# Kernel optimization log

Measured on AMD Instinct MI355X. Metric: run time of the kernel, lower is better.

Reference implementation:

```python
import jax, jax.numpy as jnp
import numpy as np

B, T, D = 4, 2048, 1024
H = 16
DK = D // H


def setup_inputs() -> dict:
    key = jax.random.key(0)
    k1, k2, k3, k4 = jax.random.split(key, 4)
    x = jax.random.normal(k1, (B, T, D), dtype=jnp.float32)
    prefix_lengths = jax.random.randint(k2, (B,), 0, 1024, dtype=jnp.int64)
    # torch Linear weights: [out_features, in_features], scaled like kaiming-uniform-ish
    W_qkv = jax.random.normal(k3, (3 * D, D), dtype=jnp.float32) / np.sqrt(D)
    W_o = jax.random.normal(k4, (D, D), dtype=jnp.float32) / np.sqrt(D)
    return {"x": x, "prefix_lengths": prefix_lengths, "W_qkv": W_qkv, "W_o": W_o}


def _prefix_lm_mask(seq_len, prefix_lengths):
    # True where attention is BLOCKED.
    pos = jnp.arange(seq_len)
    key_pos = pos[None, None, :]          # [1,1,T]
    query_pos = pos[None, :, None]        # [1,T,1]
    prefix = prefix_lengths[:, None, None]  # [B,1,1]
    q_in_pre = query_pos < prefix
    k_in_pre = key_pos < prefix
    block_pre_to_suf = q_in_pre & ~k_in_pre
    block_future_suf = ~q_in_pre & ~k_in_pre & (key_pos > query_pos)
    return block_pre_to_suf | block_future_suf  # [B,T,T]


def reference(x, prefix_lengths, W_qkv, W_o):
    Bb, Tt, Cc = x.shape
    qkv = x @ W_qkv.T                     # [B,T,3D]
    qkv = qkv.reshape(Bb, Tt, 3, H, DK).transpose(2, 0, 3, 1, 4)  # [3,B,H,T,dk]
    q, k, v = qkv[0], qkv[1], qkv[2]
    scale = 1.0 / np.sqrt(DK).astype(np.float32)
    attn = jnp.einsum('bhqd,bhkd->bhqk', q, k) * scale  # [B,H,T,T]
    pl = jnp.clip(prefix_lengths.astype(jnp.int32), 0, Tt)
    mask = _prefix_lm_mask(Tt, pl)        # [B,T,T]
    attn = jnp.where(mask[:, None, :, :], -jnp.inf, attn)
    attn = jax.nn.softmax(attn, axis=-1)
    out = jnp.einsum('bhqk,bhkd->bhqd', attn, v)  # [B,H,T,dk]
    out = out.transpose(0, 2, 1, 3).reshape(Bb, Tt, Cc)
    return out @ W_o.T
```

## Files before the change

kernel.cpp:

```cpp
#include <hip/hip_runtime.h>
#include <stdint.h>

#define NB 4
#define NT 2048
#define ND 1024
#define NH 16
#define NDK 64
#define NTD 3072

typedef __attribute__((ext_vector_type(8))) short short8;
typedef __attribute__((ext_vector_type(4))) float f32x4;
typedef unsigned short u16;
typedef unsigned int u32;

__device__ __forceinline__ u16 f2bf(float f) {
    u32 u = __builtin_bit_cast(u32, f);
    u += 0x7fffu + ((u >> 16) & 1u);
    return (u16)(u >> 16);
}
__device__ __forceinline__ float bf2f(u16 s) {
    u32 u = ((u32)s) << 16;
    return __builtin_bit_cast(float, u);
}

__device__ __forceinline__ void gl_lds16(const u16* g, u16* l) {
    __builtin_amdgcn_global_load_lds(
        (const __attribute__((address_space(1))) u32*)g,
        (__attribute__((address_space(3))) u32*)l, 16, 0, 0);
}

__device__ __forceinline__ int swz(int row, int col) {
    return row * 32 + ((((col >> 3) ^ (row >> 1) ^ (row >> 3)) & 3) << 3) + (col & 7);
}

__global__ __launch_bounds__(256) void cvt_all(const float* __restrict__ x,
                                               const float* __restrict__ wqkv,
                                               const float* __restrict__ wo,
                                               u16* __restrict__ xb,
                                               u16* __restrict__ wqb,
                                               u16* __restrict__ wob) {
    const int n0 = NB * NT * ND;
    const int n1 = 3 * ND * ND;
    int i = (blockIdx.x * 256 + threadIdx.x) * 8;
    const float* src;
    u16* dst;
    if (i < n0) {
        src = x + i; dst = xb + i;
    } else if (i < n0 + n1) {
        src = wqkv + (i - n0); dst = wqb + (i - n0);
    } else {
        src = wo + (i - n0 - n1); dst = wob + (i - n0 - n1);
    }
    float4 a = *(const float4*)(src);
    float4 b = *(const float4*)(src + 4);
    short8 r;
    r[0] = (short)f2bf(a.x); r[1] = (short)f2bf(a.y);
    r[2] = (short)f2bf(a.z); r[3] = (short)f2bf(a.w);
    r[4] = (short)f2bf(b.x); r[5] = (short)f2bf(b.y);
    r[6] = (short)f2bf(b.z); r[7] = (short)f2bf(b.w);
    *(short8*)(dst) = r;
}

template <typename OutT>
__global__ __launch_bounds__(256) void gemm_bt(const u16* __restrict__ A,
                                               const u16* __restrict__ Bm,
                                               OutT* __restrict__ C,
                                               int M, int N, int K) {
    __shared__ __align__(16) u16 As[128 * 32];
    __shared__ __align__(16) u16 Bs[128 * 32];
    const int tid  = threadIdx.x;
    const int wave = tid >> 6, lane = tid & 63;
    const int quad = lane >> 4, l16 = lane & 15;
    const int wm = wave >> 1, wn = wave & 1;
    const int row0 = blockIdx.x * 128, col0 = blockIdx.y * 128;

    f32x4 acc[4][4];
#pragma unroll
    for (int i = 0; i < 4; ++i)
#pragma unroll
        for (int j = 0; j < 4; ++j) acc[i][j] = (f32x4){0.f, 0.f, 0.f, 0.f};

    const u16* Ag = A + (size_t)(row0 + (tid >> 2)) * K + ((tid & 3) * 8);
    const u16* Bg = Bm + (size_t)(col0 + (tid >> 2)) * K + ((tid & 3) * 8);
    const size_t stride64 = (size_t)64 * K;
    u16* As0 = As + wave * 512;
    u16* As1 = As + 2048 + wave * 512;
    u16* Bs0 = Bs + wave * 512;
    u16* Bs1 = Bs + 2048 + wave * 512;

    for (int k0 = 0; k0 < K; k0 += 32) {
        gl_lds16(Ag + k0, As0);
        gl_lds16(Ag + k0 + stride64, As1);
        gl_lds16(Bg + k0, Bs0);
        gl_lds16(Bg + k0 + stride64, Bs1);
        __syncthreads();
        short8 af[4], bfr[4];
#pragma unroll
        for (int mi = 0; mi < 4; ++mi)
            af[mi] = *(const short8*)&As[(wm * 64 + mi * 16 + l16) * 32 + quad * 8];
#pragma unroll
        for (int ni = 0; ni < 4; ++ni)
            bfr[ni] = *(const short8*)&Bs[(wn * 64 + ni * 16 + l16) * 32 + quad * 8];
#pragma unroll
        for (int mi = 0; mi < 4; ++mi)
#pragma unroll
            for (int ni = 0; ni < 4; ++ni)
                acc[mi][ni] = __builtin_amdgcn_mfma_f32_16x16x32_bf16(
                    af[mi], bfr[ni], acc[mi][ni], 0, 0, 0);
        __syncthreads();
    }

#pragma unroll
    for (int mi = 0; mi < 4; ++mi) {
#pragma unroll
        for (int ni = 0; ni < 4; ++ni) {
            const int r = row0 + wm * 64 + mi * 16 + quad * 4;
            const int c = col0 + wn * 64 + ni * 16 + l16;
#pragma unroll
            for (int rr = 0; rr < 4; ++rr) {
                float v = acc[mi][ni][rr];
                if constexpr (sizeof(OutT) == 2)
                    C[(size_t)(r + rr) * N + c] = (OutT)f2bf(v);
                else
                    C[(size_t)(r + rr) * N + c] = (OutT)v;
            }
        }
    }
}

__global__ __launch_bounds__(256) void gemm_qkv(const u16* __restrict__ A,
                                                const u16* __restrict__ Bm,
                                                u16* __restrict__ Cq,
                                                u16* __restrict__ vtb) {
    const int Kd = ND, Nn = NTD;
    __shared__ __align__(16) u16 As[128 * 32];
    __shared__ __align__(16) u16 Bs[128 * 32];
    const int tid  = threadIdx.x;
    const int wave = tid >> 6, lane = tid & 63;
    const int quad = lane >> 4, l16 = lane & 15;
    const int wm = wave >> 1, wn = wave & 1;
    const int row0 = blockIdx.x * 128, col0 = blockIdx.y * 128;

    f32x4 acc[4][4];
#pragma unroll
    for (int i = 0; i < 4; ++i)
#pragma unroll
        for (int j = 0; j < 4; ++j) acc[i][j] = (f32x4){0.f, 0.f, 0.f, 0.f};

    const u16* Ag = A + (size_t)(row0 + (tid >> 2)) * Kd + ((tid & 3) * 8);
    const u16* Bg = Bm + (size_t)(col0 + (tid >> 2)) * Kd + ((tid & 3) * 8);
    const size_t stride64 = (size_t)64 * Kd;
    u16* As0 = As + wave * 512;
    u16* As1 = As + 2048 + wave * 512;
    u16* Bs0 = Bs + wave * 512;
    u16* Bs1 = Bs + 2048 + wave * 512;

    for (int k0 = 0; k0 < Kd; k0 += 32) {
        gl_lds16(Ag + k0, As0);
        gl_lds16(Ag + k0 + stride64, As1);
        gl_lds16(Bg + k0, Bs0);
        gl_lds16(Bg + k0 + stride64, Bs1);
        __syncthreads();
        short8 af[4], bfr[4];
#pragma unroll
        for (int mi = 0; mi < 4; ++mi)
            af[mi] = *(const short8*)&As[(wm * 64 + mi * 16 + l16) * 32 + quad * 8];
#pragma unroll
        for (int ni = 0; ni < 4; ++ni)
            bfr[ni] = *(const short8*)&Bs[(wn * 64 + ni * 16 + l16) * 32 + quad * 8];
#pragma unroll
        for (int mi = 0; mi < 4; ++mi)
#pragma unroll
            for (int ni = 0; ni < 4; ++ni)
                acc[mi][ni] = __builtin_amdgcn_mfma_f32_16x16x32_bf16(
                    af[mi], bfr[ni], acc[mi][ni], 0, 0, 0);
        __syncthreads();
    }

    if (col0 < 2048) {
#pragma unroll
        for (int mi = 0; mi < 4; ++mi)
#pragma unroll
            for (int ni = 0; ni < 4; ++ni) {
                const int r = row0 + wm * 64 + mi * 16 + quad * 4;
                const int c = col0 + wn * 64 + ni * 16 + l16;
#pragma unroll
                for (int rr = 0; rr < 4; ++rr)
                    Cq[(size_t)(r + rr) * Nn + c] = f2bf(acc[mi][ni][rr]);
            }
    } else {
        const int hb = ((col0 - 2048) >> 6) + wn;
        const int bq = (row0 + wm * 64) >> 11;
        const int tb = (row0 + wm * 64) & 2047;
        u16* Ovt = vtb + (size_t)(bq * NH + hb) * 64 * NT + tb;
#pragma unroll
        for (int phase = 0; phase < 2; ++phase) {
            __syncthreads();
            if ((wave >> 1) == phase) {
                u16* L = (wave & 1) ? Bs : As;
#pragma unroll
                for (int mi = 0; mi < 4; ++mi) {
                    const int r4 = mi * 4 + quad;
#pragma unroll
                    for (int ni = 0; ni < 4; ++ni) {
                        const int cl = ni * 16 + l16;
                        u32 lo = (u32)f2bf(acc[mi][ni][0]) | ((u32)f2bf(acc[mi][ni][1]) << 16);
                        u32 hi = (u32)f2bf(acc[mi][ni][2]) | ((u32)f2bf(acc[mi][ni][3]) << 16);
                        u32* p = (u32*)&L[cl * 64 + (((r4 ^ cl) & 15) << 2)];
                        p[0] = lo; p[1] = hi;
                    }
                }
#pragma unroll
                for (int rep = 0; rep < 8; ++rep) {
                    const int cl = (lane >> 3) + rep * 8;
                    const int tc = lane & 7;
                    const u32* p0 = (const u32*)&L[cl * 64 + ((((2 * tc) ^ cl) & 15) << 2)];
                    const u32* p1 = (const u32*)&L[cl * 64 + ((((2 * tc + 1) ^ cl) & 15) << 2)];
                    u32 o0 = p0[0], o1 = p0[1], o2 = p1[0], o3 = p1[1];
                    u32* q = (u32*)(Ovt + (size_t)cl * NT + tc * 8);
                    q[0] = o0; q[1] = o1; q[2] = o2; q[3] = o3;
                }
            }
        }
    }
}

#define GETREG_XCC_ID 6164
__global__ __launch_bounds__(256) void flash_prefix(const u16* __restrict__ qkv,
                                                    const u16* __restrict__ vt,
                                                    const int* __restrict__ plen,
                                                    u16* __restrict__ attn,
                                                    u32* __restrict__ ctr) {
    __shared__ __align__(16) u16 Vt2[2][2048];
    __shared__ __align__(16) u16 Kt2[2][2048];
    __shared__ __align__(16) u16 Pl[4 * 512];
    __shared__ int taskS;

    const int tid  = threadIdx.x;
    const int wave = tid >> 6, lane = tid & 63;
    const int quad = lane >> 4, l16 = lane & 15;
    const float QSCALE = 0.18033688f;
    const int ldsoff = wave * 512;

    short8 ones;
#pragma unroll
    for (int j = 0; j < 8; ++j) ones[j] = (short)0x3F80;

    const bool is64 = (plen[1] == 0) && (plen[3] == 0);
    const int xcd = (int)(__builtin_amdgcn_s_getreg(GETREG_XCC_ID) & 7);
    int q = xcd;

    for (;;) {
        if (tid == 0) taskS = (int)atomicAdd(ctr + q * 16, 1u);
        __syncthreads();
        const int pos = taskS;
        if (pos >= 256) {
            q = (q + 1) & 7;
            if (q == xcd) break;
            continue;
        }

        const int bh = (q << 3) | (pos & 7);
        const int b = bh >> 4, h = bh & 15;
        const int q0 = (31 - (pos >> 3)) * 64;

        int P = is64 ? plen[2 * b] : plen[b];
        P = P < 0 ? 0 : (P > NT ? NT : P);

        const u16* Qg = qkv + (size_t)b * NT * NTD + h * NDK;
        const u16* Kg = Qg + ND;
        const u16* Vtb = vt + (size_t)bh * 64 * NT;
        const int qbase = q0 + wave * 16;
        u16* Pw = Pl + wave * 512;

        const int vrow = tid >> 2;
        const int vtq = (tid ^ (vrow >> 1) ^ (vrow >> 3)) & 3;
        const u16* vsrc = Vtb + (size_t)vrow * NT + vtq * 8;
        const int krow = tid >> 3;
        const int kc = (tid ^ krow) & 7;
        const u16* ksrc = Kg + (size_t)krow * NTD + kc * 8;

        short8 qa[2];
#pragma unroll
        for (int kd = 0; kd < 2; ++kd) {
            short8 tq = *(const short8*)(Qg + (size_t)(qbase + l16) * NTD + kd * 32 + quad * 8);
#pragma unroll
            for (int j = 0; j < 8; ++j)
                tq[j] = (short)f2bf(bf2f((u16)tq[j]) * QSCALE);
            qa[kd] = tq;
        }

        f32x4 o[4];
#pragma unroll
        for (int nt = 0; nt < 4; ++nt) o[nt] = (f32x4){0.f, 0.f, 0.f, 0.f};
        f32x4 lsum = (f32x4){0.f, 0.f, 0.f, 0.f};

        int kl[4];
#pragma unroll
        for (int rr = 0; rr < 4; ++rr) {
            const int qrow = qbase + quad * 4 + rr;
            kl[rr] = (qrow < P) ? P : (qrow + 1);
        }
        const int klmin = (qbase < P) ? P : (qbase + 1);
        const int kmax = (q0 + 64 > P) ? (q0 + 64) : P;

        gl_lds16(vsrc, &Vt2[0][ldsoff]);
        gl_lds16(ksrc, &Kt2[0][ldsoff]);
        int buf = 0;

        for (int k0 = 0; k0 < kmax; k0 += 32) {
            __syncthreads();
            if (k0 + 32 < kmax) {
                gl_lds16(vsrc + (k0 + 32), &Vt2[buf ^ 1][ldsoff]);
                gl_lds16(ksrc + (size_t)(k0 + 32) * NTD, &Kt2[buf ^ 1][ldsoff]);
            }
            const u16* Kb = Kt2[buf];
            const u16* Vb = Vt2[buf];

            f32x4 s[2];
#pragma unroll
            for (int ni = 0; ni < 2; ++ni) {
                s[ni] = (f32x4){0.f, 0.f, 0.f, 0.f};
#pragma unroll
                for (int kd = 0; kd < 2; ++kd) {
                    const int r = ni * 16 + l16;
                    const short8 kb = *(const short8*)&Kb[r * 64 + ((((kd * 4 + quad) ^ r) & 7) << 3)];
                    s[ni] = __builtin_amdgcn_mfma_f32_16x16x32_bf16(qa[kd], kb, s[ni], 0, 0, 0);
                }
            }

            const bool full = (k0 + 32 <= klmin);
#pragma unroll
            for (int ni = 0; ni < 2; ++ni) {
#pragma unroll
                for (int rr = 0; rr < 4; ++rr) {
                    float sv = s[ni][rr];
                    if (!full) {
                        const int kpos = k0 + ni * 16 + l16;
                        sv = (kpos < kl[rr]) ? sv : -1e30f;
                    }
                    const float p = exp2f(sv);
                    const u32 u = __builtin_bit_cast(u32, p) + 0x8000u;
                    Pw[swz(quad * 4 + rr, ni * 16 + l16)] = (u16)(u >> 16);
                }
            }

            const short8 pa = *(const short8*)&Pw[swz(l16, quad * 8)];
            lsum = __builtin_amdgcn_mfma_f32_16x16x32_bf16(pa, ones, lsum, 0, 0, 0);
#pragma unroll
            for (int nt = 0; nt < 4; ++nt) {
                const short8 vb = *(const short8*)&Vb[swz(nt * 16 + l16, quad * 8)];
                o[nt] = __builtin_amdgcn_mfma_f32_16x16x32_bf16(pa, vb, o[nt], 0, 0, 0);
            }
            buf ^= 1;
        }

#pragma unroll
        for (int rr = 0; rr < 4; ++rr) {
            const float inv = 1.0f / lsum[rr];
            const size_t rowoff = (size_t)(b * NT + qbase + quad * 4 + rr) * ND + h * NDK;
#pragma unroll
            for (int nt = 0; nt < 4; ++nt)
                attn[rowoff + nt * 16 + l16] = f2bf(o[nt][rr] * inv);
        }
    }
}

extern "C" void kernel_launch(void* const* d_in, const int* in_sizes, int n_in,
                              void* d_out, int out_size, void* d_ws, size_t ws_size,
                              hipStream_t stream) {
    const float* x    = (const float*)d_in[0];
    const int*   plen = (const int*)d_in[1];
    const float* wqkv = (const float*)d_in[2];
    const float* wo   = (const float*)d_in[3];
    float* out = (float*)d_out;

    char* ws = (char*)d_ws;
    u16* xb   = (u16*)(ws);
    u16* wqb  = (u16*)(ws + 16777216);
    u16* wob  = (u16*)(ws + 23068672);
    u16* qkv  = (u16*)(ws + 25165824);
    u16* attn = (u16*)(ws + 75497472);
    u16* vtb  = (u16*)(ws + 92274688);
    u32* ctr  = (u32*)(ws + 75496960);

    hipMemsetAsync(ctr, 0, 512, stream);

    cvt_all<<<6144, 256, 0, stream>>>(x, wqkv, wo, xb, wqb, wob);

    gemm_qkv<<<dim3(64, 24), 256, 0, stream>>>(xb, wqb, qkv, vtb);

    flash_prefix<<<1024, 256, 0, stream>>>(qkv, vtb, plen, attn, ctr);

    gemm_bt<float><<<dim3(64, 8), 256, 0, stream>>>(attn, wob, out, NB * NT, ND, ND);
}
```

Before: 299.0 us.

## Transpose QK^T MFMA, prebias mask into accumulator, packed P stores, skip masked tiles

```diff
diff --git a/kernel.cpp b/kernel.cpp
--- a/kernel.cpp
+++ b/kernel.cpp
@@ -10,6 +10,7 @@
 
 typedef __attribute__((ext_vector_type(8))) short short8;
 typedef __attribute__((ext_vector_type(4))) float f32x4;
+typedef __attribute__((ext_vector_type(2))) unsigned int u32x2;
 typedef unsigned short u16;
 typedef unsigned int u32;
 
@@ -273,6 +274,11 @@
         const int qbase = q0 + wave * 16;
         u16* Pw = Pl + wave * 512;
 
+        char* const pwb = (char*)Pw + (l16 << 6);
+        u32x2* const pw0 = (u32x2*)(pwb + ((quad ^ ((l16 & 3) << 1)) << 3));
+        u32x2* const pw1 = (u32x2*)(pwb + (((4 + quad) ^ ((l16 & 3) << 1)) << 3));
+        const short8* const par = (const short8*)(pwb + ((quad ^ (l16 & 3)) << 4));
+
         const int vrow = tid >> 2;
         const int vtq = (tid ^ (vrow >> 1) ^ (vrow >> 3)) & 3;
         const u16* vsrc = Vtb + (size_t)vrow * NT + vtq * 8;
@@ -295,13 +301,10 @@
         for (int nt = 0; nt < 4; ++nt) o[nt] = (f32x4){0.f, 0.f, 0.f, 0.f};
         f32x4 lsum = (f32x4){0.f, 0.f, 0.f, 0.f};
 
-        int kl[4];
-#pragma unroll
-        for (int rr = 0; rr < 4; ++rr) {
-            const int qrow = qbase + quad * 4 + rr;
-            kl[rr] = (qrow < P) ? P : (qrow + 1);
-        }
+        const int qrow = qbase + l16;
+        const int klv  = (qrow < P) ? P : (qrow + 1);
         const int klmin = (qbase < P) ? P : (qbase + 1);
+        const int klmax = (P > qbase + 16) ? P : (qbase + 16);
         const int kmax = (q0 + 64 > P) ? (q0 + 64) : P;
 
         gl_lds16(vsrc, &Vt2[0][ldsoff]);
@@ -314,43 +317,49 @@
                 gl_lds16(vsrc + (k0 + 32), &Vt2[buf ^ 1][ldsoff]);
                 gl_lds16(ksrc + (size_t)(k0 + 32) * NTD, &Kt2[buf ^ 1][ldsoff]);
             }
-            const u16* Kb = Kt2[buf];
-            const u16* Vb = Vt2[buf];
-
-            f32x4 s[2];
-#pragma unroll
-            for (int ni = 0; ni < 2; ++ni) {
-                s[ni] = (f32x4){0.f, 0.f, 0.f, 0.f};
-#pragma unroll
-                for (int kd = 0; kd < 2; ++kd) {
-                    const int r = ni * 16 + l16;
-                    const short8 kb = *(const short8*)&Kb[r * 64 + ((((kd * 4 + quad) ^ r) & 7) << 3)];
-                    s[ni] = __builtin_amdgcn_mfma_f32_16x16x32_bf16(qa[kd], kb, s[ni], 0, 0, 0);
+            if (k0 < klmax) {
+                const u16* Kb = Kt2[buf];
+                const u16* Vb = Vt2[buf];
+
+                const bool full = (k0 + 32 <= klmin);
+                f32x4 s[2];
+#pragma unroll
+                for (int ni = 0; ni < 2; ++ni) {
+                    if (full) {
+                        s[ni] = (f32x4){0.f, 0.f, 0.f, 0.f};
+                    } else {
+#pragma unroll
+                        for (int rr = 0; rr < 4; ++rr)
+                            s[ni][rr] = (k0 + ni * 16 + quad * 4 + rr < klv) ? 0.f : -1e30f;
+                    }
+#pragma unroll
+                    for (int kd = 0; kd < 2; ++kd) {
+                        const int r = ni * 16 + l16;
+                        const short8 kb = *(const short8*)&Kb[r * 64 + ((((kd * 4 + quad) ^ r) & 7) << 3)];
+                        s[ni] = __builtin_amdgcn_mfma_f32_16x16x32_bf16(kb, qa[kd], s[ni], 0, 0, 0);
+                    }
                 }
-            }
-
-            const bool full = (k0 + 32 <= klmin);
-#pragma unroll
-            for (int ni = 0; ni < 2; ++ni) {
-#pragma unroll
-                for (int rr = 0; rr < 4; ++rr) {
-                    float sv = s[ni][rr];
-                    if (!full) {
-                        const int kpos = k0 + ni * 16 + l16;
-                        sv = (kpos < kl[rr]) ? sv : -1e30f;
-                    }
-                    const float p = exp2f(sv);
-                    const u32 u = __builtin_bit_cast(u32, p) + 0x8000u;
-                    Pw[swz(quad * 4 + rr, ni * 16 + l16)] = (u16)(u >> 16);
+
+#pragma unroll
+                for (int ni = 0; ni < 2; ++ni) {
+                    const float p0 = exp2f(s[ni][0]);
+                    const float p1 = exp2f(s[ni][1]);
+                    const float p2 = exp2f(s[ni][2]);
+                    const float p3 = exp2f(s[ni][3]);
+                    u32 w0, w1;
+                    asm("v_cvt_pk_bf16_f32 %0, %1, %2" : "=v"(w0) : "v"(p0), "v"(p1));
+                    asm("v_cvt_pk_bf16_f32 %0, %1, %2" : "=v"(w1) : "v"(p2), "v"(p3));
+                    u32x2 wv; wv[0] = w0; wv[1] = w1;
+                    *(ni ? pw1 : pw0) = wv;
                 }
-            }
-
-            const short8 pa = *(const short8*)&Pw[swz(l16, quad * 8)];
-            lsum = __builtin_amdgcn_mfma_f32_16x16x32_bf16(pa, ones, lsum, 0, 0, 0);
-#pragma unroll
-            for (int nt = 0; nt < 4; ++nt) {
-                const short8 vb = *(const short8*)&Vb[swz(nt * 16 + l16, quad * 8)];
-                o[nt] = __builtin_amdgcn_mfma_f32_16x16x32_bf16(pa, vb, o[nt], 0, 0, 0);
+
+                const short8 pa = *par;
+                lsum = __builtin_amdgcn_mfma_f32_16x16x32_bf16(pa, ones, lsum, 0, 0, 0);
+#pragma unroll
+                for (int nt = 0; nt < 4; ++nt) {
+                    const short8 vb = *(const short8*)&Vb[swz(nt * 16 + l16, quad * 8)];
+                    o[nt] = __builtin_amdgcn_mfma_f32_16x16x32_bf16(pa, vb, o[nt], 0, 0, 0);
+                }
             }
             buf ^= 1;
         }
@@ -390,7 +399,7 @@
 
     gemm_qkv<<<dim3(64, 24), 256, 0, stream>>>(xb, wqb, qkv, vtb);
 
-    flash_prefix<<<1024, 256, 0, stream>>>(qkv, vtb, plen, attn, ctr);
+    flash_prefix<<<2048, 256, 0, stream>>>(qkv, vtb, plen, attn, ctr);
 
     gemm_bt<float><<<dim3(64, 8), 256, 0, stream>>>(attn, wob, out, NB * NT, ND, ND);
 }
```

After: 313.6 us. 4.9% more time.
